# Kernel tuning notes

Measured on AMD Instinct MI355X. Metric: run time of the kernel, lower is better.

## Reference

```python
import jax, jax.numpy as jnp
import numpy as np

N_GROUPS = 4
N_LIMITED_GROUPS = 2
TOP_K = 2
ROUTE_SCALE = 1.0


def setup_inputs() -> dict:
    key = jax.random.key(0)
    k1, k2, k3, k4 = jax.random.split(key, 4)
    n_tokens, dim, n_experts = 65536, 4096, 16
    return {
        "x": jax.random.normal(k1, (n_tokens, dim), dtype=jnp.float32),
        "w1_weight": jax.random.normal(k2, (n_experts, dim), dtype=jnp.float32) * 0.02,
        "w1_bias": jax.random.normal(k3, (n_experts,), dtype=jnp.float32) * 0.02,
        "route_bias": jax.random.normal(k4, (n_experts,), dtype=jnp.float32) * 0.02,
    }


def reference(x, w1_weight, w1_bias, route_bias):
    # Linear scorer: [N, E]
    logits = x @ w1_weight.T + w1_bias
    # softmax in fp32 (score_func == 'softmax')
    scores = jax.nn.softmax(logits.astype(jnp.float32), axis=-1)
    # bias add (moe_use_bias=True); original_scores includes the bias
    scores = scores + route_bias
    original_scores = scores

    n = x.shape[0]
    # group masking: view [N, n_groups, experts_per_group]
    g = scores.reshape(n, N_GROUPS, -1)
    group_scores = g.max(axis=-1)  # amax path since bias is not None
    _, gidx = jax.lax.top_k(group_scores, N_LIMITED_GROUPS)  # [N, n_limited]
    keep = jnp.zeros((n, N_GROUPS), dtype=bool).at[
        jnp.arange(n)[:, None], gidx
    ].set(True)
    masked = jnp.where(keep[:, :, None], g, -jnp.inf).reshape(n, -1)

    # top-k over masked scores; gather values from original (unmasked-at-topk) scores
    _, indices = jax.lax.top_k(masked, TOP_K)  # [N, k]
    values = jnp.take_along_axis(original_scores, indices, axis=1) * ROUTE_SCALE
    return values.astype(x.dtype), indices
```

## Files before the change

kernel.cpp:

```cpp
#include <hip/hip_runtime.h>
#include <math.h>

constexpr int NE = 16;
constexpr int NG = 4;
#define MARGIN 1e-4

typedef __attribute__((ext_vector_type(8))) short bf16x8;
typedef __attribute__((ext_vector_type(4))) float f32x4;

__device__ __forceinline__ unsigned short f2bf_rne(float f) {
    unsigned u = __float_as_uint(f);
    unsigned r = (u + 0x7fffu + ((u >> 16) & 1u)) >> 16;
    return (unsigned short)r;
}

__device__ __forceinline__ void gload_lds16(const float* g, float* l) {
    __builtin_amdgcn_global_load_lds(
        (const __attribute__((address_space(1))) void*)g,
        (__attribute__((address_space(3))) void*)l, 16, 0, 0);
}

__global__ __launch_bounds__(256)
void w_prep_kernel(const float* __restrict__ w, float* __restrict__ wt,
                   unsigned short* __restrict__ whi, unsigned short* __restrict__ wlo,
                   int dim, int n) {
    int id = blockIdx.x * 256 + threadIdx.x;
    if (id < n) {
        int e = id / dim;
        int k = id - e * dim;
        float f = w[id];
        wt[(size_t)k * NE + e] = f;
        unsigned short h = f2bf_rne(f);
        float back = __uint_as_float(((unsigned)h) << 16);
        whi[id] = h;
        wlo[id] = f2bf_rne(f - back);
    }
}

struct RouteR { double v1, v2; int i1, i2; double mg, mo, ms; };

__device__ __forceinline__ RouteR route_epilogue(const double* tot,
                                                 const float* w1b,
                                                 const float* rbias)
{
    double logit[NE];
    double m = -INFINITY;
#pragma unroll
    for (int e = 0; e < NE; ++e) {
        logit[e] = tot[e] + (double)w1b[e];
        m = fmax(m, logit[e]);
    }
    double ssum = 0.0, p[NE];
#pragma unroll
    for (int e = 0; e < NE; ++e) { p[e] = exp(logit[e] - m); ssum += p[e]; }
    double inv = 1.0 / ssum, sc[NE];
#pragma unroll
    for (int e = 0; e < NE; ++e) sc[e] = p[e] * inv + (double)rbias[e];

    double gm[NG];
#pragma unroll
    for (int g = 0; g < NG; ++g) {
        double a = fmax(sc[g * 4 + 0], sc[g * 4 + 1]);
        double b = fmax(sc[g * 4 + 2], sc[g * 4 + 3]);
        gm[g] = fmax(a, b);
    }
    int g1 = 0;
#pragma unroll
    for (int g = 1; g < NG; ++g) if (gm[g] > gm[g1]) g1 = g;
    int g2 = (g1 == 0) ? 1 : 0;
#pragma unroll
    for (int g = 0; g < NG; ++g) if (g != g1 && gm[g] > gm[g2]) g2 = g;
    double gm3 = -INFINITY;
#pragma unroll
    for (int g = 0; g < NG; ++g)
        if (g != g1 && g != g2 && gm[g] > gm3) gm3 = gm[g];

    RouteR r;
    r.v1 = -INFINITY; r.i1 = 0;
#pragma unroll
    for (int e = 0; e < NE; ++e) {
        int g = e >> 2;
        bool keep = (g == g1) || (g == g2);
        if (keep && sc[e] > r.v1) { r.v1 = sc[e]; r.i1 = e; }
    }
    r.v2 = -INFINITY; r.i2 = 0;
#pragma unroll
    for (int e = 0; e < NE; ++e) {
        int g = e >> 2;
        bool keep = ((g == g1) || (g == g2)) && (e != r.i1);
        if (keep && sc[e] > r.v2) { r.v2 = sc[e]; r.i2 = e; }
    }
    double v3 = -INFINITY;
#pragma unroll
    for (int e = 0; e < NE; ++e) {
        int g = e >> 2;
        bool keep = ((g == g1) || (g == g2)) && (e != r.i1) && (e != r.i2);
        if (keep && sc[e] > v3) v3 = sc[e];
    }
    r.mg = gm[g2] - gm3;
    r.mo = r.v1 - r.v2;
    r.ms = r.v2 - v3;
    return r;
}

__global__ __launch_bounds__(256)
void k1_mfma(const float* __restrict__ x,
             const unsigned short* __restrict__ whi,
             const unsigned short* __restrict__ wlo,
             const float* __restrict__ w1b,
             const float* __restrict__ rbias,
             float* __restrict__ dout,
             int* __restrict__ fcount,
             int* __restrict__ flist,
             int n_tokens, int dim)
{
    __shared__ float tile[2][16][260];
    const int tid  = threadIdx.x;
    const int uw   = __builtin_amdgcn_readfirstlane(tid >> 6);
    const int lane = tid & 63;
    const int m    = lane & 15;
    const int kg   = lane >> 4;
    const long tok0 = (long)blockIdx.x * 16;
    const int nst = dim / 256;

    const unsigned short* whp = whi + (size_t)m * dim + uw * 64 + kg * 8;
    const unsigned short* wlp = wlo + (size_t)m * dim + uw * 64 + kg * 8;

    f32x4 acc = {0.f, 0.f, 0.f, 0.f};

    bf16x8 bh0 = *(const bf16x8*)(whp);
    bf16x8 bh1 = *(const bf16x8*)(whp + 32);
    bf16x8 bl0 = *(const bf16x8*)(wlp);
    bf16x8 bl1 = *(const bf16x8*)(wlp + 32);
#pragma unroll
    for (int i = 0; i < 4; ++i)
        gload_lds16(x + (tok0 + uw * 4 + i) * (size_t)dim + lane * 4,
                    &tile[0][uw * 4 + i][0]);

    int cur = 0;
    for (int s = 0; s < nst; ++s) {
        bf16x8 nbh0 = bh0, nbh1 = bh1, nbl0 = bl0, nbl1 = bl1;
        if (s + 1 < nst) {
            const unsigned short* wh2 = whp + (size_t)(s + 1) * 256;
            const unsigned short* wl2 = wlp + (size_t)(s + 1) * 256;
            nbh0 = *(const bf16x8*)(wh2);
            nbh1 = *(const bf16x8*)(wh2 + 32);
            nbl0 = *(const bf16x8*)(wl2);
            nbl1 = *(const bf16x8*)(wl2 + 32);
#pragma unroll
            for (int i = 0; i < 4; ++i)
                gload_lds16(x + (tok0 + uw * 4 + i) * (size_t)dim
                              + (size_t)(s + 1) * 256 + lane * 4,
                            &tile[cur ^ 1][uw * 4 + i][0]);
            __builtin_amdgcn_sched_barrier(0);
            asm volatile("s_waitcnt vmcnt(8)" ::: "memory");
            __builtin_amdgcn_sched_barrier(0);
        } else {
            __builtin_amdgcn_sched_barrier(0);
            asm volatile("s_waitcnt vmcnt(0)" ::: "memory");
            __builtin_amdgcn_sched_barrier(0);
        }
        __builtin_amdgcn_s_barrier();
        __builtin_amdgcn_sched_barrier(0);

#pragma unroll
        for (int it = 0; it < 2; ++it) {
            const float* ap = &tile[cur][m][uw * 64 + kg * 8 + it * 32];
            float4 xa = *(const float4*)ap;
            float4 xb = *(const float4*)(ap + 4);
            float xf[8] = {xa.x, xa.y, xa.z, xa.w, xb.x, xb.y, xb.z, xb.w};
            bf16x8 xhi, xlo;
#pragma unroll
            for (int j = 0; j < 8; ++j) {
                float f = xf[j];
                unsigned short h = f2bf_rne(f);
                float back = __uint_as_float(((unsigned)h) << 16);
                xhi[j] = (short)h;
                xlo[j] = (short)f2bf_rne(f - back);
            }
            bf16x8 wh = it ? bh1 : bh0;
            bf16x8 wl = it ? bl1 : bl0;
            acc = __builtin_amdgcn_mfma_f32_16x16x32_bf16(xhi, wh, acc, 0, 0, 0);
            acc = __builtin_amdgcn_mfma_f32_16x16x32_bf16(xlo, wh, acc, 0, 0, 0);
            acc = __builtin_amdgcn_mfma_f32_16x16x32_bf16(xhi, wl, acc, 0, 0, 0);
        }
        __builtin_amdgcn_sched_barrier(0);
        __builtin_amdgcn_s_barrier();
        __builtin_amdgcn_sched_barrier(0);
        bh0 = nbh0; bh1 = nbh1; bl0 = nbl0; bl1 = nbl1;
        cur ^= 1;
    }

    float (*red)[16][17] = (float (*)[16][17])(&tile[0][0][0]);
#pragma unroll
    for (int j = 0; j < 4; ++j)
        red[uw][kg * 4 + j][m] = acc[j];
    __syncthreads();

    if (uw == 0 && lane < 16) {
        double tot[NE];
#pragma unroll
        for (int e = 0; e < NE; ++e)
            tot[e] = (((double)red[0][lane][e] + (double)red[1][lane][e])
                      + (double)red[2][lane][e]) + (double)red[3][lane][e];
        RouteR r = route_epilogue(tot, w1b, rbias);
        long tok = tok0 + lane;

        double mmin = fmin(r.mg, fmin(r.mo, r.ms));
        if (mmin < MARGIN) {
            int idx = atomicAdd(fcount, 1);
            if (idx < n_tokens) flist[idx] = (int)tok;
        }
        float2 vv; vv.x = (float)r.v1; vv.y = (float)r.v2;
        *(float2*)(dout + tok * 2) = vv;
        float2 iv; iv.x = (float)r.i1; iv.y = (float)r.i2;
        *(float2*)(dout + (long)n_tokens * 2 + tok * 2) = iv;
    }
}

__global__ __launch_bounds__(256)
void k2_recheck(const float* __restrict__ x,
                const float* __restrict__ wt,
                const float* __restrict__ w1b,
                const float* __restrict__ rbias,
                float* __restrict__ dout,
                const int* __restrict__ fcount,
                const int* __restrict__ flist,
                int n_tokens, int dim)
{
    const int tid  = threadIdx.x;
    const int lane = tid & 63;
    const int wavesPerBlock = blockDim.x >> 6;
    const int wglobal = blockIdx.x * wavesPerBlock + (tid >> 6);
    const int nwaves  = gridDim.x * wavesPerBlock;
    int nf = *fcount;
    if (nf > n_tokens) nf = n_tokens;
    const int nq = dim / 256;

    for (int i = wglobal; i < nf; i += nwaves) {
        const int t = flist[i];
        const float* xr = x + (size_t)t * dim;

        double part[NE];
#pragma unroll
        for (int e = 0; e < NE; ++e) part[e] = 0.0;

        for (int q = 0; q < nq; ++q) {
            float4 xv = *(const float4*)(xr + q * 256 + lane * 4);
#pragma unroll
            for (int j = 0; j < 4; ++j) {
                int k = q * 256 + lane * 4 + j;
                double xd = (double)((const float*)&xv)[j];
                const float* wr = wt + (size_t)k * NE;
#pragma unroll
                for (int e = 0; e < NE; ++e)
                    part[e] = fma(xd, (double)wr[e], part[e]);
            }
        }

#pragma unroll
        for (int off = 1; off < 64; off <<= 1) {
#pragma unroll
            for (int e = 0; e < NE; ++e)
                part[e] += __shfl_xor(part[e], off, 64);
        }

        RouteR r = route_epilogue(part, w1b, rbias);
        if (lane == 0) {
            float2 vv; vv.x = (float)r.v1; vv.y = (float)r.v2;
            *(float2*)(dout + (long)t * 2) = vv;
            float2 iv; iv.x = (float)r.i1; iv.y = (float)r.i2;
            *(float2*)(dout + (long)n_tokens * 2 + (long)t * 2) = iv;
        }
    }
}

__global__ __launch_bounds__(256)
void router_fallback(const float* __restrict__ x,
                     const float* __restrict__ w1w,
                     const float* __restrict__ w1b,
                     const float* __restrict__ rbias,
                     float* __restrict__ dout,
                     int n_tokens, int dim)
{
    __shared__ double wbuf4[4][16][NE];
    const int tid  = threadIdx.x;
    const int uwid = __builtin_amdgcn_readfirstlane(tid >> 6);
    const int lane = tid & 63;
    const int slice = dim / 4;
    const int nst  = slice / 16;
    const long tokA = (long)blockIdx.x * 128 + lane;
    const long tokB = tokA + 64;
    const float* xA = x + tokA * (size_t)dim + (size_t)uwid * slice;
    const float* xB = x + tokB * (size_t)dim + (size_t)uwid * slice;

    double accA[NE], accB[NE];
#pragma unroll
    for (int e = 0; e < NE; ++e) { accA[e] = 0.0; accB[e] = 0.0; }

    float4 a0 = *(const float4*)(xA + 0), a1 = *(const float4*)(xA + 4);
    float4 a2 = *(const float4*)(xA + 8), a3 = *(const float4*)(xA + 12);
    float4 b0 = *(const float4*)(xB + 0), b1 = *(const float4*)(xB + 4);
    float4 b2 = *(const float4*)(xB + 8), b3 = *(const float4*)(xB + 12);
    float4 wreg;
    {
        const int i0 = lane * 4;
#pragma unroll
        for (int j = 0; j < 4; ++j) {
            int i = i0 + j;
            ((float*)&wreg)[j] = w1w[(size_t)(i & 15) * dim + uwid * slice + (i >> 4)];
        }
    }

    for (int c = 0; c < nst; ++c) {
        {
            double* dst = &wbuf4[uwid][0][0] + lane * 4;
            dst[0] = (double)wreg.x;  dst[1] = (double)wreg.y;
            dst[2] = (double)wreg.z;  dst[3] = (double)wreg.w;
        }
        float4 na0=a0,na1=a1,na2=a2,na3=a3,nb0=b0,nb1=b1,nb2=b2,nb3=b3;
        if (c + 1 < nst) {
            const float* pa = xA + (c + 1) * 16;
            const float* pb = xB + (c + 1) * 16;
            na0 = *(const float4*)(pa + 0);  na1 = *(const float4*)(pa + 4);
            na2 = *(const float4*)(pa + 8);  na3 = *(const float4*)(pa + 12);
            nb0 = *(const float4*)(pb + 0);  nb1 = *(const float4*)(pb + 4);
            nb2 = *(const float4*)(pb + 8);  nb3 = *(const float4*)(pb + 12);
            const int kb = uwid * slice + (c + 1) * 16;
            const int i0 = lane * 4;
#pragma unroll
            for (int j = 0; j < 4; ++j) {
                int i = i0 + j;
                ((float*)&wreg)[j] = w1w[(size_t)(i & 15) * dim + kb + (i >> 4)];
            }
        }
        float fa[16], fb[16];
        fa[0]=a0.x; fa[1]=a0.y; fa[2]=a0.z; fa[3]=a0.w;
        fa[4]=a1.x; fa[5]=a1.y; fa[6]=a1.z; fa[7]=a1.w;
        fa[8]=a2.x; fa[9]=a2.y; fa[10]=a2.z; fa[11]=a2.w;
        fa[12]=a3.x; fa[13]=a3.y; fa[14]=a3.z; fa[15]=a3.w;
        fb[0]=b0.x; fb[1]=b0.y; fb[2]=b0.z; fb[3]=b0.w;
        fb[4]=b1.x; fb[5]=b1.y; fb[6]=b1.z; fb[7]=b1.w;
        fb[8]=b2.x; fb[9]=b2.y; fb[10]=b2.z; fb[11]=b2.w;
        fb[12]=b3.x; fb[13]=b3.y; fb[14]=b3.z; fb[15]=b3.w;
#pragma unroll
        for (int kk = 0; kk < 16; ++kk) {
            double xa_ = (double)fa[kk];
            double xb_ = (double)fb[kk];
#pragma unroll
            for (int ep = 0; ep < NE / 2; ++ep) {
                double2 wv = *(const double2*)&wbuf4[uwid][kk][ep * 2];
                accA[ep*2+0] = fma(xa_, wv.x, accA[ep*2+0]);
                accA[ep*2+1] = fma(xa_, wv.y, accA[ep*2+1]);
                accB[ep*2+0] = fma(xb_, wv.x, accB[ep*2+0]);
                accB[ep*2+1] = fma(xb_, wv.y, accB[ep*2+1]);
            }
        }
        a0=na0; a1=na1; a2=na2; a3=na3;
        b0=nb0; b1=nb1; b2=nb2; b3=nb3;
    }

    __syncthreads();
    __shared__ double red[3][2][64][NE + 1];
    if (uwid != 0) {
#pragma unroll
        for (int e = 0; e < NE; ++e) {
            red[uwid - 1][0][lane][e] = accA[e];
            red[uwid - 1][1][lane][e] = accB[e];
        }
    }
    __syncthreads();
    if (uwid != 0) return;

#pragma unroll
    for (int t = 0; t < 2; ++t) {
        double tot[NE];
#pragma unroll
        for (int e = 0; e < NE; ++e) {
            double a = (t == 0) ? accA[e] : accB[e];
            tot[e] = ((a + red[0][t][lane][e]) + red[1][t][lane][e])
                     + red[2][t][lane][e];
        }
        RouteR r = route_epilogue(tot, w1b, rbias);
        long tok = (t == 0) ? tokA : tokB;
        float2 vv; vv.x = (float)r.v1; vv.y = (float)r.v2;
        *(float2*)(dout + tok * 2) = vv;
        float2 iv; iv.x = (float)r.i1; iv.y = (float)r.i2;
        *(float2*)(dout + (long)n_tokens * 2 + tok * 2) = iv;
    }
}

extern "C" void kernel_launch(void* const* d_in, const int* in_sizes, int n_in,
                              void* d_out, int out_size, void* d_ws, size_t ws_size,
                              hipStream_t stream)
{
    const float* x   = (const float*)d_in[0];
    const float* w1w = (const float*)d_in[1];
    const float* w1b = (const float*)d_in[2];
    const float* rb  = (const float*)d_in[3];
    float* out = (float*)d_out;

    const int ne       = in_sizes[2];
    const int dim      = in_sizes[1] / ne;
    const int n_tokens = in_sizes[0] / dim;

    const int nW = dim * ne;
    const size_t WT_BYTES  = (size_t)nW * sizeof(float);
    const size_t WHI_OFF   = WT_BYTES;
    const size_t WLO_OFF   = WHI_OFF + (size_t)nW * 2;
    const size_t COUNT_OFF = WLO_OFF + (size_t)nW * 2;
    const size_t LIST_OFF  = COUNT_OFF + 128;
    const size_t need = LIST_OFF + (size_t)n_tokens * sizeof(int);

    if (ws_size >= need) {
        float* wt            = (float*)d_ws;
        unsigned short* whi  = (unsigned short*)((char*)d_ws + WHI_OFF);
        unsigned short* wlo  = (unsigned short*)((char*)d_ws + WLO_OFF);
        int* fcount          = (int*)((char*)d_ws + COUNT_OFF);
        int* flist           = (int*)((char*)d_ws + LIST_OFF);

        hipMemsetAsync(fcount, 0, sizeof(int), stream);
        hipLaunchKernelGGL(w_prep_kernel, dim3((nW + 255) / 256), dim3(256),
                           0, stream, w1w, wt, whi, wlo, dim, nW);
        hipLaunchKernelGGL(k1_mfma, dim3(n_tokens / 16), dim3(256),
                           0, stream, x, whi, wlo, w1b, rb, out, fcount, flist,
                           n_tokens, dim);
        hipLaunchKernelGGL(k2_recheck, dim3(256), dim3(256),
                           0, stream, x, wt, w1b, rb, out, fcount, flist,
                           n_tokens, dim);
    } else {
        hipLaunchKernelGGL(router_fallback, dim3(n_tokens / 128), dim3(256),
                           0, stream, x, w1w, w1b, rb, out, n_tokens, dim);
    }
}
```

Baseline: 271.0 us.

## Give each wave its own 16-token tile over full K, dropping block barriers

Before, the four waves of a block split the K dimension of one 16-token tile, which forced two block-wide barriers per K step and a cross-wave LDS reduction at the end. Now each wave processes its own 16 tokens over the whole K range with a private double-buffered 64-column LDS tile using an XOR swizzle, so the block barriers and the reduction go away and the grid handles 64 tokens per block. The cost is more K steps per wave with smaller loads, and each wave now has to read the full weight stream itself. Removing the per-wave reduction also changes the fp64 accumulation order before the epilogue.

```diff
diff --git a/kernel.cpp b/kernel.cpp
--- a/kernel.cpp
+++ b/kernel.cpp
@@ -114,17 +114,36 @@
              int* __restrict__ flist,
              int n_tokens, int dim)
 {
-    __shared__ float tile[2][16][260];
+    __shared__ float tiles[4][2][16][64];
+    __shared__ float scl[4][16][NE + 1];
+
     const int tid  = threadIdx.x;
     const int uw   = __builtin_amdgcn_readfirstlane(tid >> 6);
     const int lane = tid & 63;
     const int m    = lane & 15;
     const int kg   = lane >> 4;
-    const long tok0 = (long)blockIdx.x * 16;
-    const int nst = dim / 256;
-
-    const unsigned short* whp = whi + (size_t)m * dim + uw * 64 + kg * 8;
-    const unsigned short* wlp = wlo + (size_t)m * dim + uw * 64 + kg * 8;
+    const int h    = lane >> 4;
+    const int sl   = lane & 15;
+    const long tok0 = (long)blockIdx.x * 64 + uw * 16;
+    const int nst = dim / 64;
+
+    size_t srcoff[4];
+#pragma unroll
+    for (int i = 0; i < 4; ++i) {
+        int r = 4 * i + h;
+        srcoff[i] = (size_t)(tok0 + r) * dim + ((sl ^ (r & 7)) << 2);
+    }
+
+    const unsigned short* whp = whi + (size_t)m * dim + kg * 8;
+    const unsigned short* wlp = wlo + (size_t)m * dim + kg * 8;
+
+    int rd[2][2];
+#pragma unroll
+    for (int it = 0; it < 2; ++it) {
+        int s0 = it * 8 + 2 * kg;
+        rd[it][0] = ((s0)     ^ (m & 7)) << 2;
+        rd[it][1] = ((s0 + 1) ^ (m & 7)) << 2;
+    }
 
     f32x4 acc = {0.f, 0.f, 0.f, 0.f};
 
@@ -134,24 +153,22 @@
     bf16x8 bl1 = *(const bf16x8*)(wlp + 32);
 #pragma unroll
     for (int i = 0; i < 4; ++i)
-        gload_lds16(x + (tok0 + uw * 4 + i) * (size_t)dim + lane * 4,
-                    &tile[0][uw * 4 + i][0]);
+        gload_lds16(x + srcoff[i], &tiles[uw][0][4 * i][0]);
 
     int cur = 0;
     for (int s = 0; s < nst; ++s) {
         bf16x8 nbh0 = bh0, nbh1 = bh1, nbl0 = bl0, nbl1 = bl1;
         if (s + 1 < nst) {
-            const unsigned short* wh2 = whp + (size_t)(s + 1) * 256;
-            const unsigned short* wl2 = wlp + (size_t)(s + 1) * 256;
+            const unsigned short* wh2 = whp + (size_t)(s + 1) * 64;
+            const unsigned short* wl2 = wlp + (size_t)(s + 1) * 64;
             nbh0 = *(const bf16x8*)(wh2);
             nbh1 = *(const bf16x8*)(wh2 + 32);
             nbl0 = *(const bf16x8*)(wl2);
             nbl1 = *(const bf16x8*)(wl2 + 32);
 #pragma unroll
             for (int i = 0; i < 4; ++i)
-                gload_lds16(x + (tok0 + uw * 4 + i) * (size_t)dim
-                              + (size_t)(s + 1) * 256 + lane * 4,
-                            &tile[cur ^ 1][uw * 4 + i][0]);
+                gload_lds16(x + srcoff[i] + (size_t)(s + 1) * 64,
+                            &tiles[uw][cur ^ 1][4 * i][0]);
             __builtin_amdgcn_sched_barrier(0);
             asm volatile("s_waitcnt vmcnt(8)" ::: "memory");
             __builtin_amdgcn_sched_barrier(0);
@@ -160,22 +177,19 @@
             asm volatile("s_waitcnt vmcnt(0)" ::: "memory");
             __builtin_amdgcn_sched_barrier(0);
         }
-        __builtin_amdgcn_s_barrier();
-        __builtin_amdgcn_sched_barrier(0);
 
 #pragma unroll
         for (int it = 0; it < 2; ++it) {
-            const float* ap = &tile[cur][m][uw * 64 + kg * 8 + it * 32];
-            float4 xa = *(const float4*)ap;
-            float4 xb = *(const float4*)(ap + 4);
+            float4 xa = *(const float4*)&tiles[uw][cur][m][rd[it][0]];
+            float4 xb = *(const float4*)&tiles[uw][cur][m][rd[it][1]];
             float xf[8] = {xa.x, xa.y, xa.z, xa.w, xb.x, xb.y, xb.z, xb.w};
             bf16x8 xhi, xlo;
 #pragma unroll
             for (int j = 0; j < 8; ++j) {
                 float f = xf[j];
-                unsigned short h = f2bf_rne(f);
-                float back = __uint_as_float(((unsigned)h) << 16);
-                xhi[j] = (short)h;
+                unsigned short hh = f2bf_rne(f);
+                float back = __uint_as_float(((unsigned)hh) << 16);
+                xhi[j] = (short)hh;
                 xlo[j] = (short)f2bf_rne(f - back);
             }
             bf16x8 wh = it ? bh1 : bh0;
@@ -184,25 +198,18 @@
             acc = __builtin_amdgcn_mfma_f32_16x16x32_bf16(xlo, wh, acc, 0, 0, 0);
             acc = __builtin_amdgcn_mfma_f32_16x16x32_bf16(xhi, wl, acc, 0, 0, 0);
         }
-        __builtin_amdgcn_sched_barrier(0);
-        __builtin_amdgcn_s_barrier();
-        __builtin_amdgcn_sched_barrier(0);
         bh0 = nbh0; bh1 = nbh1; bl0 = nbl0; bl1 = nbl1;
         cur ^= 1;
     }
 
-    float (*red)[16][17] = (float (*)[16][17])(&tile[0][0][0]);
 #pragma unroll
     for (int j = 0; j < 4; ++j)
-        red[uw][kg * 4 + j][m] = acc[j];
-    __syncthreads();
-
-    if (uw == 0 && lane < 16) {
+        scl[uw][kg * 4 + j][m] = acc[j];
+
+    if (lane < 16) {
         double tot[NE];
 #pragma unroll
-        for (int e = 0; e < NE; ++e)
-            tot[e] = (((double)red[0][lane][e] + (double)red[1][lane][e])
-                      + (double)red[2][lane][e]) + (double)red[3][lane][e];
+        for (int e = 0; e < NE; ++e) tot[e] = (double)scl[uw][lane][e];
         RouteR r = route_epilogue(tot, w1b, rbias);
         long tok = tok0 + lane;
 
@@ -422,7 +429,7 @@
         hipMemsetAsync(fcount, 0, sizeof(int), stream);
         hipLaunchKernelGGL(w_prep_kernel, dim3((nW + 255) / 256), dim3(256),
                            0, stream, w1w, wt, whi, wlo, dim, nW);
-        hipLaunchKernelGGL(k1_mfma, dim3(n_tokens / 16), dim3(256),
+        hipLaunchKernelGGL(k1_mfma, dim3(n_tokens / 64), dim3(256),
                            0, stream, x, whi, wlo, w1b, rb, out, fcount, flist,
                            n_tokens, dim);
         hipLaunchKernelGGL(k2_recheck, dim3(256), dim3(256),
```

Result: slower. 280.2 us, median of 2 (+3.4%).

## Replace direct global-to-LDS loads with register-staged prefetch pipeline

Applied to the files above, without the earlier changes.

Drops the global_load_lds direct-to-LDS copies of x. Each stage's x tile is now loaded into registers two stages ahead and written into the alternate LDS buffer after the MFMAs, with one barrier per stage instead of two. This aims to cut barrier overhead and the explicit vmcnt waits, and to let loads overlap compute more deeply. In exchange it uses extra VGPRs and adds LDS write instructions, and the compiler inserts its own waits on the register loads.

```diff
diff --git a/kernel.cpp b/kernel.cpp
--- a/kernel.cpp
+++ b/kernel.cpp
@@ -12,12 +12,6 @@
     unsigned u = __float_as_uint(f);
     unsigned r = (u + 0x7fffu + ((u >> 16) & 1u)) >> 16;
     return (unsigned short)r;
-}
-
-__device__ __forceinline__ void gload_lds16(const float* g, float* l) {
-    __builtin_amdgcn_global_load_lds(
-        (const __attribute__((address_space(1))) void*)g,
-        (__attribute__((address_space(3))) void*)l, 16, 0, 0);
 }
 
 __global__ __launch_bounds__(256)
@@ -126,43 +120,40 @@
     const unsigned short* whp = whi + (size_t)m * dim + uw * 64 + kg * 8;
     const unsigned short* wlp = wlo + (size_t)m * dim + uw * 64 + kg * 8;
 
+    const float* xrow[4];
+#pragma unroll
+    for (int i = 0; i < 4; ++i)
+        xrow[i] = x + (tok0 + uw * 4 + i) * (size_t)dim + lane * 4;
+
     f32x4 acc = {0.f, 0.f, 0.f, 0.f};
 
+    float4 st[4];
+#pragma unroll
+    for (int i = 0; i < 4; ++i) st[i] = *(const float4*)(xrow[i]);
     bf16x8 bh0 = *(const bf16x8*)(whp);
     bf16x8 bh1 = *(const bf16x8*)(whp + 32);
     bf16x8 bl0 = *(const bf16x8*)(wlp);
     bf16x8 bl1 = *(const bf16x8*)(wlp + 32);
+
 #pragma unroll
     for (int i = 0; i < 4; ++i)
-        gload_lds16(x + (tok0 + uw * 4 + i) * (size_t)dim + lane * 4,
-                    &tile[0][uw * 4 + i][0]);
+        *(float4*)&tile[0][uw * 4 + i][lane * 4] = st[i];
+
+    bf16x8 nbh0 = bh0, nbh1 = bh1, nbl0 = bl0, nbl1 = bl1;
+    if (nst > 1) {
+#pragma unroll
+        for (int i = 0; i < 4; ++i)
+            st[i] = *(const float4*)(xrow[i] + 256);
+        nbh0 = *(const bf16x8*)(whp + 256);
+        nbh1 = *(const bf16x8*)(whp + 256 + 32);
+        nbl0 = *(const bf16x8*)(wlp + 256);
+        nbl1 = *(const bf16x8*)(wlp + 256 + 32);
+    }
+    asm volatile("s_waitcnt lgkmcnt(0)" ::: "memory");
+    __builtin_amdgcn_s_barrier();
 
     int cur = 0;
     for (int s = 0; s < nst; ++s) {
-        bf16x8 nbh0 = bh0, nbh1 = bh1, nbl0 = bl0, nbl1 = bl1;
-        if (s + 1 < nst) {
-            const unsigned short* wh2 = whp + (size_t)(s + 1) * 256;
-            const unsigned short* wl2 = wlp + (size_t)(s + 1) * 256;
-            nbh0 = *(const bf16x8*)(wh2);
-            nbh1 = *(const bf16x8*)(wh2 + 32);
-            nbl0 = *(const bf16x8*)(wl2);
-            nbl1 = *(const bf16x8*)(wl2 + 32);
-#pragma unroll
-            for (int i = 0; i < 4; ++i)
-                gload_lds16(x + (tok0 + uw * 4 + i) * (size_t)dim
-                              + (size_t)(s + 1) * 256 + lane * 4,
-                            &tile[cur ^ 1][uw * 4 + i][0]);
-            __builtin_amdgcn_sched_barrier(0);
-            asm volatile("s_waitcnt vmcnt(8)" ::: "memory");
-            __builtin_amdgcn_sched_barrier(0);
-        } else {
-            __builtin_amdgcn_sched_barrier(0);
-            asm volatile("s_waitcnt vmcnt(0)" ::: "memory");
-            __builtin_amdgcn_sched_barrier(0);
-        }
-        __builtin_amdgcn_s_barrier();
-        __builtin_amdgcn_sched_barrier(0);
-
 #pragma unroll
         for (int it = 0; it < 2; ++it) {
             const float* ap = &tile[cur][m][uw * 64 + kg * 8 + it * 32];
@@ -173,9 +164,9 @@
 #pragma unroll
             for (int j = 0; j < 8; ++j) {
                 float f = xf[j];
-                unsigned short h = f2bf_rne(f);
-                float back = __uint_as_float(((unsigned)h) << 16);
-                xhi[j] = (short)h;
+                unsigned short hh = f2bf_rne(f);
+                float back = __uint_as_float(((unsigned)hh) << 16);
+                xhi[j] = (short)hh;
                 xlo[j] = (short)f2bf_rne(f - back);
             }
             bf16x8 wh = it ? bh1 : bh0;
@@ -184,11 +175,26 @@
             acc = __builtin_amdgcn_mfma_f32_16x16x32_bf16(xlo, wh, acc, 0, 0, 0);
             acc = __builtin_amdgcn_mfma_f32_16x16x32_bf16(xhi, wl, acc, 0, 0, 0);
         }
-        __builtin_amdgcn_sched_barrier(0);
-        __builtin_amdgcn_s_barrier();
-        __builtin_amdgcn_sched_barrier(0);
-        bh0 = nbh0; bh1 = nbh1; bl0 = nbl0; bl1 = nbl1;
-        cur ^= 1;
+
+        if (s + 1 < nst) {
+#pragma unroll
+            for (int i = 0; i < 4; ++i)
+                *(float4*)&tile[cur ^ 1][uw * 4 + i][lane * 4] = st[i];
+            bh0 = nbh0; bh1 = nbh1; bl0 = nbl0; bl1 = nbl1;
+            if (s + 2 < nst) {
+                const size_t off = (size_t)(s + 2) * 256;
+#pragma unroll
+                for (int i = 0; i < 4; ++i)
+                    st[i] = *(const float4*)(xrow[i] + off);
+                nbh0 = *(const bf16x8*)(whp + off);
+                nbh1 = *(const bf16x8*)(whp + off + 32);
+                nbl0 = *(const bf16x8*)(wlp + off);
+                nbl1 = *(const bf16x8*)(wlp + off + 32);
+            }
+            asm volatile("s_waitcnt lgkmcnt(0)" ::: "memory");
+            __builtin_amdgcn_s_barrier();
+            cur ^= 1;
+        }
     }
 
     float (*red)[16][17] = (float (*)[16][17])(&tile[0][0][0]);
```

Result: slower. 490.7 us (+81.0%).
